# Kernel tuning notes

Hardware: AMD Instinct MI355X
Metric: run time of the kernel (lower is better)

## Reference

```python
import jax, jax.numpy as jnp
import numpy as np

_EPS = 1e-6
B, N, W, R, NW = 64, 1024, 64, 4, 1


def _cosine_weights(memory, keys, strengths):
    # memory: [B,N,W], keys: [B,H,W], strengths: [B,H] -> [B,H,N]
    dot = jnp.einsum('bhw,bnw->bhn', keys, memory)
    mem_norm = jnp.sqrt(jnp.sum(memory * memory, axis=-1) + _EPS)  # [B,N]
    key_norm = jnp.sqrt(jnp.sum(keys * keys, axis=-1) + _EPS)      # [B,H]
    sim = dot / (key_norm[:, :, None] * mem_norm[:, None, :] + _EPS)
    sharp = sim * jax.nn.softplus(strengths)[:, :, None]
    return jax.nn.softmax(sharp, axis=-1)


def _allocation(usage):
    # usage: [B,N] -> allocation weights [B,N] (DNC sort-based free-list)
    usage = _EPS + (1.0 - _EPS) * usage
    nonusage = 1.0 - usage
    sorted_nonusage, indices = jax.lax.top_k(nonusage, N)
    sorted_usage = 1.0 - sorted_nonusage
    prod_excl = jnp.concatenate(
        [jnp.ones_like(sorted_usage[:, :1]), jnp.cumprod(sorted_usage[:, :-1], axis=-1)], axis=-1)
    sorted_alloc = sorted_nonusage * prod_excl
    inv_perm = jnp.argsort(indices, axis=-1)  # batch_invert_permutation
    return jnp.take_along_axis(sorted_alloc, inv_perm, axis=-1)  # batch_gather


def _forward(memory, prev_read_weights, prev_write_weights, prev_usage, prev_link,
             prev_precedence, read_keys, read_strengths, write_keys, write_strengths,
             write_vectors, erase_vectors, free_gate, alloc_gate, write_gate, read_mode):
    # ---- usage update (Freeness.call); prev write weights are stop-gradient'd ----
    ww = jax.lax.stop_gradient(prev_write_weights)
    agg_write = 1.0 - jnp.prod(1.0 - ww, axis=1)                       # [B,N]
    usage = prev_usage + (1.0 - prev_usage) * agg_write
    phi = jnp.prod(1.0 - free_gate[:, :, None] * prev_read_weights, axis=1)
    usage = usage * phi
    # ---- write weights: content + allocation ----
    write_content = _cosine_weights(memory, write_keys, write_strengths)  # [B,NW,N]
    wg = alloc_gate * write_gate                                          # [B,NW]
    allocs = []
    u = usage
    for i in range(NW):  # fixed small head loop
        a = _allocation(u)
        allocs.append(a)
        u = u + (1.0 - u) * wg[:, i:i + 1] * a
    alloc_w = jnp.stack(allocs, axis=1)                                   # [B,NW,N]
    ag = alloc_gate[:, :, None]
    write_weights = write_gate[:, :, None] * (ag * alloc_w + (1.0 - ag) * write_content)
    # ---- erase + write memory ----
    reset = jnp.prod(1.0 - write_weights[:, :, :, None] * erase_vectors[:, :, None, :], axis=1)
    memory_new = memory * reset + jnp.einsum('bwn,bwk->bnk', write_weights, write_vectors)
    # ---- temporal link matrix update ----
    wi = write_weights[:, :, :, None]   # [B,NW,N,1]
    wj = write_weights[:, :, None, :]   # [B,NW,1,N]
    new_link = (1.0 - wi - wj) * prev_link + wi * prev_precedence[:, :, None, :]
    link = new_link * (1.0 - jnp.eye(N, dtype=memory.dtype))[None, None]  # zero diagonal
    # (precedence update, part of new state; not needed for read_words output)
    precedence = (1.0 - jnp.sum(write_weights, axis=-1, keepdims=True)) * prev_precedence + write_weights
    del precedence
    # ---- read weights: content + directional (forward/backward along link) ----
    read_content = _cosine_weights(memory_new, read_keys, read_strengths)   # [B,R,N]
    fwd_w = jnp.einsum('brm,bwnm->brwn', prev_read_weights, link)           # adjoint_b=True
    bwd_w = jnp.einsum('brm,bwmn->brwn', prev_read_weights, link)
    mode = jax.nn.softmax(read_mode, axis=-1)                                # [B,R,2*NW+1]
    backward_mode = mode[:, :, :NW]
    forward_mode = mode[:, :, NW:2 * NW]
    content_mode = mode[:, :, 2 * NW]
    read_weights = (content_mode[:, :, None] * read_content
                    + jnp.einsum('brw,brwn->brn', forward_mode, fwd_w)
                    + jnp.einsum('brw,brwn->brn', backward_mode, bwd_w))
    read_words = jnp.einsum('brn,bnw->brw', read_weights, memory_new)        # [B,R,W]
    return read_words


def setup_inputs() -> dict:
    key = jax.random.key(0)
    ks = jax.random.split(key, 16)
    rn = lambda k, s: jax.random.normal(k, s, jnp.float32)
    ru = lambda k, s: jax.random.uniform(k, s, dtype=jnp.float32)
    return {
        'memory': rn(ks[0], (B, N, W)),
        'prev_read_weights': ru(ks[1], (B, R, N)),
        'prev_write_weights': ru(ks[2], (B, NW, N)),
        'prev_usage': ru(ks[3], (B, N)),
        'prev_link': ru(ks[4], (B, NW, N, N)),
        'prev_precedence': ru(ks[5], (B, NW, N)),
        'read_keys': rn(ks[6], (B, R, W)),
        'read_strengths': rn(ks[7], (B, R)),
        'write_keys': rn(ks[8], (B, NW, W)),
        'write_strengths': rn(ks[9], (B, NW)),
        'write_vectors': rn(ks[10], (B, NW, W)),
        'erase_vectors': ru(ks[11], (B, NW, W)),
        'free_gate': ru(ks[12], (B, R)),
        'alloc_gate': ru(ks[13], (B, NW)),
        'write_gate': ru(ks[14], (B, NW)),
        'read_mode': rn(ks[15], (B, R, 2 * NW + 1)),
    }


def reference(memory, prev_read_weights, prev_write_weights, prev_usage, prev_link,
              prev_precedence, read_keys, read_strengths, write_keys, write_strengths,
              write_vectors, erase_vectors, free_gate, alloc_gate, write_gate, read_mode):
    return _forward(memory, prev_read_weights, prev_write_weights, prev_usage, prev_link,
                    prev_precedence, read_keys, read_strengths, write_keys, write_strengths,
                    write_vectors, erase_vectors, free_gate, alloc_gate, write_gate, read_mode)
```

## Files before the change

### kernel.cpp

```cpp
#include <hip/hip_runtime.h>
#include <cmath>

#define NN 1024
#define BB 64
#define WD 64
#define RR 4

constexpr float EPSF = 1e-6f;

__device__ __forceinline__ float softplusf(float x) {
    return fmaxf(x, 0.f) + log1pf(expf(-fabsf(x)));
}

__device__ __forceinline__ float block_sum(float v, float* red, float* bc) {
#pragma unroll
    for (int o = 1; o < 64; o <<= 1) v += __shfl_xor(v, o, 64);
    const int wid = threadIdx.x >> 6, lane = threadIdx.x & 63;
    if (lane == 0) red[wid] = v;
    __syncthreads();
    if (wid == 0) {
        float x = (lane < 16) ? red[lane] : 0.f;
#pragma unroll
        for (int o = 1; o < 16; o <<= 1) x += __shfl_xor(x, o, 64);
        if (lane == 0) bc[0] = x;
    }
    __syncthreads();
    return bc[0];
}

__device__ __forceinline__ float block_max(float v, float* red, float* bc) {
#pragma unroll
    for (int o = 1; o < 64; o <<= 1) v = fmaxf(v, __shfl_xor(v, o, 64));
    const int wid = threadIdx.x >> 6, lane = threadIdx.x & 63;
    if (lane == 0) red[wid] = v;
    __syncthreads();
    if (wid == 0) {
        float x = (lane < 16) ? red[lane] : -INFINITY;
#pragma unroll
        for (int o = 1; o < 16; o <<= 1) x = fmaxf(x, __shfl_xor(x, o, 64));
        if (lane == 0) bc[0] = x;
    }
    __syncthreads();
    return bc[0];
}

__device__ __forceinline__ float4 block_sum4(float4 v, float4* red, float4* bc) {
#pragma unroll
    for (int o = 1; o < 64; o <<= 1) {
        v.x += __shfl_xor(v.x, o, 64); v.y += __shfl_xor(v.y, o, 64);
        v.z += __shfl_xor(v.z, o, 64); v.w += __shfl_xor(v.w, o, 64);
    }
    const int wid = threadIdx.x >> 6, lane = threadIdx.x & 63;
    if (lane == 0) red[wid] = v;
    __syncthreads();
    if (wid == 0) {
        float4 x;
        if (lane < 16) x = red[lane];
        else { x.x = 0.f; x.y = 0.f; x.z = 0.f; x.w = 0.f; }
#pragma unroll
        for (int o = 1; o < 16; o <<= 1) {
            x.x += __shfl_xor(x.x, o, 64); x.y += __shfl_xor(x.y, o, 64);
            x.z += __shfl_xor(x.z, o, 64); x.w += __shfl_xor(x.w, o, 64);
        }
        if (lane == 0) bc[0] = x;
    }
    __syncthreads();
    return bc[0];
}

__device__ __forceinline__ float4 block_max4(float4 v, float4* red, float4* bc) {
#pragma unroll
    for (int o = 1; o < 64; o <<= 1) {
        v.x = fmaxf(v.x, __shfl_xor(v.x, o, 64)); v.y = fmaxf(v.y, __shfl_xor(v.y, o, 64));
        v.z = fmaxf(v.z, __shfl_xor(v.z, o, 64)); v.w = fmaxf(v.w, __shfl_xor(v.w, o, 64));
    }
    const int wid = threadIdx.x >> 6, lane = threadIdx.x & 63;
    if (lane == 0) red[wid] = v;
    __syncthreads();
    if (wid == 0) {
        float4 x;
        if (lane < 16) x = red[lane];
        else { x.x = -INFINITY; x.y = -INFINITY; x.z = -INFINITY; x.w = -INFINITY; }
#pragma unroll
        for (int o = 1; o < 16; o <<= 1) {
            x.x = fmaxf(x.x, __shfl_xor(x.x, o, 64)); x.y = fmaxf(x.y, __shfl_xor(x.y, o, 64));
            x.z = fmaxf(x.z, __shfl_xor(x.z, o, 64)); x.w = fmaxf(x.w, __shfl_xor(x.w, o, 64));
        }
        if (lane == 0) bc[0] = x;
    }
    __syncthreads();
    return bc[0];
}

__global__ __launch_bounds__(1024) void prep_kernel(
    const float* __restrict__ memory, const float* __restrict__ prw,
    const float* __restrict__ pww, const float* __restrict__ pusage,
    const float* __restrict__ pprec,
    const float* __restrict__ rkeys_g, const float* __restrict__ rstr_g,
    const float* __restrict__ wkeys_g, const float* __restrict__ wstr_g,
    const float* __restrict__ wvec_g, const float* __restrict__ evec_g,
    const float* __restrict__ fg_g, const float* __restrict__ ag_g,
    const float* __restrict__ wg_g,
    float* __restrict__ wwG, float* __restrict__ rcG,
    float* __restrict__ SrpG, float* __restrict__ SuwwG)
{
    __shared__ float wkey[WD], wvecS[WD], evecS[WD], rkey[RR * WD];
    __shared__ float skey[NN];
    __shared__ int   sidx[NN];
    __shared__ float pArr[NN], wcArr[NN], allocArr[NN];
    __shared__ float red1[16], bc1[1];
    __shared__ float4 red4[16], bc4[1];

    const int b = blockIdx.x, tid = threadIdx.x, n = tid;

    if (tid < WD) {
        wkey[tid]  = wkeys_g[b * WD + tid];
        wvecS[tid] = wvec_g[b * WD + tid];
        evecS[tid] = evec_g[b * WD + tid];
    } else if (tid >= 128 && tid < 128 + RR * WD) {
        int k = tid - 128;
        rkey[k] = rkeys_g[b * RR * WD + k];
    }
    __syncthreads();

    float ur[RR];
#pragma unroll
    for (int r = 0; r < RR; ++r) ur[r] = prw[((size_t)b * RR + r) * NN + n];
    const float pw = pww[b * NN + n];
    const float pu = pusage[b * NN + n];
    float usage = pu + (1.f - pu) * pw;
    float phi = 1.f;
#pragma unroll
    for (int r = 0; r < RR; ++r) phi *= (1.f - fg_g[b * RR + r] * ur[r]);
    usage *= phi;

    const float* mrow = memory + ((size_t)b * NN + n) * WD;
    float dot = 0.f, nrm = 0.f, knrm = 0.f;
#pragma unroll 4
    for (int w4 = 0; w4 < WD / 4; ++w4) {
        const float4 m = *(const float4*)(mrow + w4 * 4);
        const float4 k = *(const float4*)(wkey + w4 * 4);
        dot  += m.x * k.x + m.y * k.y + m.z * k.z + m.w * k.w;
        nrm  += m.x * m.x + m.y * m.y + m.z * m.z + m.w * m.w;
        knrm += k.x * k.x + k.y * k.y + k.z * k.z + k.w * k.w;
    }
    const float sim = dot / (sqrtf(knrm + EPSF) * sqrtf(nrm + EPSF) + EPSF);
    const float sharp = sim * softplusf(wstr_g[b]);
    const float mxw = block_max(sharp, red1, bc1);
    const float exw = expf(sharp - mxw);
    const float smw = block_sum(exw, red1, bc1);
    wcArr[n] = exw / smw;

    const float ue = EPSF + (1.f - EPSF) * usage;
    skey[n] = 1.f - ue;
    sidx[n] = n;
    __syncthreads();
    for (int k = 2; k <= NN; k <<= 1) {
        for (int j = k >> 1; j > 0; j >>= 1) {
            const int ixj = tid ^ j;
            if (ixj > tid) {
                const float ka = skey[tid], kb = skey[ixj];
                const int ia = sidx[tid], ib = sidx[ixj];
                const bool precBA = (kb > ka) || (kb == ka && ib < ia);
                const bool precAB = (ka > kb) || (ka == kb && ia < ib);
                const bool dosw = ((tid & k) == 0) ? precBA : precAB;
                if (dosw) { skey[tid] = kb; skey[ixj] = ka; sidx[tid] = ib; sidx[ixj] = ia; }
            }
            __syncthreads();
        }
    }
    pArr[n] = (n == 0) ? 1.f : (1.f - skey[n - 1]);
    __syncthreads();
    for (int off = 1; off < NN; off <<= 1) {
        const float t = (n >= off) ? pArr[n - off] : 1.f;
        __syncthreads();
        pArr[n] *= t;
        __syncthreads();
    }
    allocArr[sidx[n]] = skey[n] * pArr[n];
    __syncthreads();

    const float agv = ag_g[b], wgv = wg_g[b];
    const float ww = wgv * (agv * allocArr[n] + (1.f - agv) * wcArr[n]);
    wwG[b * NN + n] = ww;

    float rdot0 = 0, rdot1 = 0, rdot2 = 0, rdot3 = 0, nn2 = 0;
    float rk0 = 0, rk1 = 0, rk2 = 0, rk3 = 0;
#pragma unroll 4
    for (int w4 = 0; w4 < WD / 4; ++w4) {
        const float4 m = *(const float4*)(mrow + w4 * 4);
        const float4 e = *(const float4*)(evecS + w4 * 4);
        const float4 v = *(const float4*)(wvecS + w4 * 4);
        float4 mn_;
        mn_.x = m.x * (1.f - ww * e.x) + ww * v.x;
        mn_.y = m.y * (1.f - ww * e.y) + ww * v.y;
        mn_.z = m.z * (1.f - ww * e.z) + ww * v.z;
        mn_.w = m.w * (1.f - ww * e.w) + ww * v.w;
        nn2 += mn_.x * mn_.x + mn_.y * mn_.y + mn_.z * mn_.z + mn_.w * mn_.w;
        const float4 k0 = *(const float4*)(rkey + 0 * WD + w4 * 4);
        const float4 k1 = *(const float4*)(rkey + 1 * WD + w4 * 4);
        const float4 k2 = *(const float4*)(rkey + 2 * WD + w4 * 4);
        const float4 k3 = *(const float4*)(rkey + 3 * WD + w4 * 4);
        rdot0 += k0.x * mn_.x + k0.y * mn_.y + k0.z * mn_.z + k0.w * mn_.w;
        rdot1 += k1.x * mn_.x + k1.y * mn_.y + k1.z * mn_.z + k1.w * mn_.w;
        rdot2 += k2.x * mn_.x + k2.y * mn_.y + k2.z * mn_.z + k2.w * mn_.w;
        rdot3 += k3.x * mn_.x + k3.y * mn_.y + k3.z * mn_.z + k3.w * mn_.w;
        rk0 += k0.x * k0.x + k0.y * k0.y + k0.z * k0.z + k0.w * k0.w;
        rk1 += k1.x * k1.x + k1.y * k1.y + k1.z * k1.z + k1.w * k1.w;
        rk2 += k2.x * k2.x + k2.y * k2.y + k2.z * k2.z + k2.w * k2.w;
        rk3 += k3.x * k3.x + k3.y * k3.y + k3.z * k3.z + k3.w * k3.w;
    }
    const float mnn = sqrtf(nn2 + EPSF);
    float4 sharp4;
    sharp4.x = rdot0 / (sqrtf(rk0 + EPSF) * mnn + EPSF) * softplusf(rstr_g[b * RR + 0]);
    sharp4.y = rdot1 / (sqrtf(rk1 + EPSF) * mnn + EPSF) * softplusf(rstr_g[b * RR + 1]);
    sharp4.z = rdot2 / (sqrtf(rk2 + EPSF) * mnn + EPSF) * softplusf(rstr_g[b * RR + 2]);
    sharp4.w = rdot3 / (sqrtf(rk3 + EPSF) * mnn + EPSF) * softplusf(rstr_g[b * RR + 3]);
    const float4 mx4 = block_max4(sharp4, red4, bc4);
    float4 e4;
    e4.x = expf(sharp4.x - mx4.x); e4.y = expf(sharp4.y - mx4.y);
    e4.z = expf(sharp4.z - mx4.z); e4.w = expf(sharp4.w - mx4.w);
    const float4 s4 = block_sum4(e4, red4, bc4);
    rcG[((size_t)b * RR + 0) * NN + n] = e4.x / s4.x;
    rcG[((size_t)b * RR + 1) * NN + n] = e4.y / s4.y;
    rcG[((size_t)b * RR + 2) * NN + n] = e4.z / s4.z;
    rcG[((size_t)b * RR + 3) * NN + n] = e4.w / s4.w;

    const float prec_n = pprec[b * NN + n];
    float4 sp4, sw4;
    sp4.x = ur[0] * prec_n; sp4.y = ur[1] * prec_n; sp4.z = ur[2] * prec_n; sp4.w = ur[3] * prec_n;
    const float4 SrpV = block_sum4(sp4, red4, bc4);
    sw4.x = ur[0] * ww; sw4.y = ur[1] * ww; sw4.z = ur[2] * ww; sw4.w = ur[3] * ww;
    const float4 SuwwV = block_sum4(sw4, red4, bc4);
    if (tid == 0) {
        SrpG[b * RR + 0] = SrpV.x; SrpG[b * RR + 1] = SrpV.y;
        SrpG[b * RR + 2] = SrpV.z; SrpG[b * RR + 3] = SrpV.w;
        SuwwG[b * RR + 0] = SuwwV.x; SuwwG[b * RR + 1] = SuwwV.y;
        SuwwG[b * RR + 2] = SuwwV.z; SuwwG[b * RR + 3] = SuwwV.w;
    }
}

__global__ __launch_bounds__(256) void link_kernel(
    const float* __restrict__ L, const float* __restrict__ prw,
    const float* __restrict__ wwG,
    float* __restrict__ rowU, float* __restrict__ rowV,
    float* __restrict__ colU, float* __restrict__ colV)
{
    __shared__ float uL[RR * NN];
    __shared__ float uwL[RR * NN];
    __shared__ float tile[64 * 68];

    const int b = blockIdx.y;
    const int n0 = blockIdx.x * 64;
    const int t = threadIdx.x;
    const int lane = t & 63;
    const int wid = t >> 6;

    for (int k = t; k < RR * NN; k += 256) {
        const float u = prw[(size_t)b * RR * NN + k];
        uL[k] = u;
        uwL[k] = u * wwG[b * NN + (k & (NN - 1))];
    }
    __syncthreads();

    const float* Lb = L + (size_t)b * NN * NN;
    float fuA = 0.f, fvA = 0.f;

    for (int tIdx = 0; tIdx < 16; ++tIdx) {
        const int m0 = tIdx * 64;
#pragma unroll
        for (int k = 0; k < 4; ++k) {
            const int f4 = t + k * 256;
            const int row = f4 >> 4, c4 = f4 & 15;
            const float4 v = *(const float4*)&Lb[(size_t)(n0 + row) * NN + m0 + c4 * 4];
            *(float4*)&tile[row * 68 + c4 * 4] = v;
        }
        __syncthreads();

#pragma unroll 4
        for (int g = 0; g < 16; ++g) {
            const float4 v  = *(const float4*)&tile[lane * 68 + g * 4];
            const float4 u  = *(const float4*)&uL[wid * NN + m0 + g * 4];
            const float4 uw = *(const float4*)&uwL[wid * NN + m0 + g * 4];
            fuA += v.x * u.x + v.y * u.y + v.z * u.z + v.w * u.w;
            fvA += v.x * uw.x + v.y * uw.y + v.z * uw.z + v.w * uw.w;
        }

        float cu = 0.f, cv = 0.f;
#pragma unroll 4
        for (int n4 = 0; n4 < 16; ++n4) {
            const float4 u  = *(const float4*)&uL[wid * NN + n0 + n4 * 4];
            const float4 uw = *(const float4*)&uwL[wid * NN + n0 + n4 * 4];
            const float v0 = tile[(n4 * 4 + 0) * 68 + lane];
            const float v1 = tile[(n4 * 4 + 1) * 68 + lane];
            const float v2 = tile[(n4 * 4 + 2) * 68 + lane];
            const float v3 = tile[(n4 * 4 + 3) * 68 + lane];
            cu += v0 * u.x + v1 * u.y + v2 * u.z + v3 * u.w;
            cv += v0 * uw.x + v1 * uw.y + v2 * uw.z + v3 * uw.w;
        }
        unsafeAtomicAdd(&colU[((size_t)b * RR + wid) * NN + m0 + lane], cu);
        unsafeAtomicAdd(&colV[((size_t)b * RR + wid) * NN + m0 + lane], cv);
        __syncthreads();
    }
    rowU[((size_t)b * RR + wid) * NN + n0 + lane] = fuA;
    rowV[((size_t)b * RR + wid) * NN + n0 + lane] = fvA;
}

__global__ __launch_bounds__(256) void combine_kernel(
    const float* __restrict__ memory, const float* __restrict__ prw,
    const float* __restrict__ pprec, const float* __restrict__ L,
    const float* __restrict__ evec_g, const float* __restrict__ wvec_g,
    const float* __restrict__ rmode_g,
    const float* __restrict__ wwG, const float* __restrict__ rcG,
    const float* __restrict__ rowU, const float* __restrict__ rowV,
    const float* __restrict__ colU, const float* __restrict__ colV,
    const float* __restrict__ SrpG, const float* __restrict__ SuwwG,
    float* __restrict__ out)
{
    __shared__ float rwL[RR][256];
    __shared__ float wwS[256];

    const int b = blockIdx.y;
    const int n0 = blockIdx.x * 256;
    const int t = threadIdx.x;
    const int n = n0 + t;

    const float wwn = wwG[b * NN + n];
    wwS[t] = wwn;
    const float prec_n = pprec[b * NN + n];
    const float diag = L[(size_t)b * NN * NN + (size_t)n * (NN + 1)];

#pragma unroll
    for (int r = 0; r < RR; ++r) {
        const size_t idx = ((size_t)b * RR + r) * NN + n;
        const float un = prw[idx];
        const float rc = rcG[idx];
        const float ru = rowU[idx], rv = rowV[idx];
        const float cuv = colU[idx], cvv = colV[idx];
        const float Srp = SrpG[b * RR + r], Suww = SuwwG[b * RR + r];
        const float corr = un * (1.f - 2.f * wwn) * diag;
        const float fwd = (1.f - wwn) * ru - rv - corr + wwn * (Srp - un * prec_n);
        const float bwd = (1.f - wwn) * cuv - cvv - corr + prec_n * (Suww - un * wwn);
        const float m0 = rmode_g[((size_t)b * RR + r) * 3 + 0];
        const float m1 = rmode_g[((size_t)b * RR + r) * 3 + 1];
        const float m2 = rmode_g[((size_t)b * RR + r) * 3 + 2];
        const float mx = fmaxf(m0, fmaxf(m1, m2));
        const float e0 = expf(m0 - mx), e1 = expf(m1 - mx), e2 = expf(m2 - mx);
        const float inv = 1.f / (e0 + e1 + e2);
        rwL[r][t] = (e2 * inv) * rc + (e1 * inv) * fwd + (e0 * inv) * bwd;
    }
    __syncthreads();

    const int r = t >> 6, w = t & 63;
    const float ev = evec_g[b * WD + w], wv = wvec_g[b * WD + w];
    float acc = 0.f;
    const float* mb = memory + ((size_t)b * NN + n0) * WD;
#pragma unroll 8
    for (int i = 0; i < 256; ++i) {
        const float m = mb[(size_t)i * WD + w];
        const float wwi = wwS[i];
        const float mn_ = m * (1.f - wwi * ev) + wwi * wv;
        acc += rwL[r][i] * mn_;
    }
    unsafeAtomicAdd(&out[((size_t)b * RR + r) * WD + w], acc);
}

extern "C" void kernel_launch(void* const* d_in, const int* in_sizes, int n_in,
                              void* d_out, int out_size, void* d_ws, size_t ws_size,
                              hipStream_t stream) {
    const float* memory = (const float*)d_in[0];
    const float* prw    = (const float*)d_in[1];
    const float* pww    = (const float*)d_in[2];
    const float* pusage = (const float*)d_in[3];
    const float* plink  = (const float*)d_in[4];
    const float* pprec  = (const float*)d_in[5];
    const float* rkeys  = (const float*)d_in[6];
    const float* rstr   = (const float*)d_in[7];
    const float* wkeys  = (const float*)d_in[8];
    const float* wstr   = (const float*)d_in[9];
    const float* wvec   = (const float*)d_in[10];
    const float* evec   = (const float*)d_in[11];
    const float* fg     = (const float*)d_in[12];
    const float* ag     = (const float*)d_in[13];
    const float* wg     = (const float*)d_in[14];
    const float* rmode  = (const float*)d_in[15];

    float* ws = (float*)d_ws;
    const size_t BN  = (size_t)BB * NN;
    const size_t BRN = (size_t)BB * RR * NN;
    float* wwG  = ws;
    float* rcG  = wwG + BN;
    float* rowU = rcG + BRN;
    float* rowV = rowU + BRN;
    float* colU = rowV + BRN;
    float* colV = colU + BRN;
    float* Srp  = colV + BRN;
    float* Suww = Srp + (size_t)BB * RR;

    hipMemsetAsync(colU, 0, 2 * BRN * sizeof(float), stream);
    hipMemsetAsync(d_out, 0, (size_t)out_size * sizeof(float), stream);

    prep_kernel<<<BB, 1024, 0, stream>>>(memory, prw, pww, pusage, pprec,
                                         rkeys, rstr, wkeys, wstr, wvec, evec,
                                         fg, ag, wg, wwG, rcG, Srp, Suww);
    link_kernel<<<dim3(16, BB), 256, 0, stream>>>(plink, prw, wwG,
                                                  rowU, rowV, colU, colV);
    combine_kernel<<<dim3(4, BB), 256, 0, stream>>>(memory, prw, pprec, plink,
                                                    evec, wvec, rmode,
                                                    wwG, rcG, rowU, rowV, colU, colV,
                                                    Srp, Suww, (float*)d_out);
}
```

Baseline: 600.0 us.

## Split link kernel across column quarters with register prefetch and smaller LDS

The link kernel now splits each row block into four column ranges, raising the grid from 16 to 64 blocks per batch. It shrinks the u/uw shared buffers to the slices each block needs, and uses atomics for the row partial sums (the buffers are now zeroed by memset). It also prefetches the next L tile into registers while computing on the current one. It reorganises column sums as float4 partials with a cross-lane shuffle reduction, and precomputes u*ww in the prep kernel. The combine kernel is split into more, smaller blocks for parallelism. The cost is more atomics and extra global traffic for uwG.

```diff
diff --git a/kernel.cpp b/kernel.cpp
--- a/kernel.cpp
+++ b/kernel.cpp
@@ -101,7 +101,7 @@
     const float* __restrict__ wvec_g, const float* __restrict__ evec_g,
     const float* __restrict__ fg_g, const float* __restrict__ ag_g,
     const float* __restrict__ wg_g,
-    float* __restrict__ wwG, float* __restrict__ rcG,
+    float* __restrict__ wwG, float* __restrict__ uwG, float* __restrict__ rcG,
     float* __restrict__ SrpG, float* __restrict__ SuwwG)
 {
     __shared__ float wkey[WD], wvecS[WD], evecS[WD], rkey[RR * WD];
@@ -183,6 +183,9 @@
     const float agv = ag_g[b], wgv = wg_g[b];
     const float ww = wgv * (agv * allocArr[n] + (1.f - agv) * wcArr[n]);
     wwG[b * NN + n] = ww;
+#pragma unroll
+    for (int r = 0; r < RR; ++r)
+        uwG[((size_t)b * RR + r) * NN + n] = ur[r] * ww;
 
     float rdot0 = 0, rdot1 = 0, rdot2 = 0, rdot3 = 0, nn2 = 0;
     float rk0 = 0, rk1 = 0, rk2 = 0, rk3 = 0;
@@ -240,70 +243,113 @@
     }
 }
 
-__global__ __launch_bounds__(256) void link_kernel(
-    const float* __restrict__ L, const float* __restrict__ prw,
-    const float* __restrict__ wwG,
+__global__ __launch_bounds__(256, 4) void link_kernel(
+    const float* __restrict__ L, const float* __restrict__ uG,
+    const float* __restrict__ uwG,
     float* __restrict__ rowU, float* __restrict__ rowV,
     float* __restrict__ colU, float* __restrict__ colV)
 {
-    __shared__ float uL[RR * NN];
-    __shared__ float uwL[RR * NN];
+    __shared__ float uRow[RR * 256];
+    __shared__ float uwRow[RR * 256];
+    __shared__ float uCol[RR * 64];
+    __shared__ float uwCol[RR * 64];
     __shared__ float tile[64 * 68];
 
     const int b = blockIdx.y;
-    const int n0 = blockIdx.x * 64;
+    const int bx = blockIdx.x;
+    const int n0 = (bx >> 2) * 64;
+    const int mBase = (bx & 3) * 256;
     const int t = threadIdx.x;
     const int lane = t & 63;
     const int wid = t >> 6;
 
-    for (int k = t; k < RR * NN; k += 256) {
-        const float u = prw[(size_t)b * RR * NN + k];
-        uL[k] = u;
-        uwL[k] = u * wwG[b * NN + (k & (NN - 1))];
-    }
-    __syncthreads();
-
-    const float* Lb = L + (size_t)b * NN * NN;
+#pragma unroll
+    for (int k = 0; k < 4; ++k) {
+        const int kk = t + (k << 8);
+        const int r = kk >> 8, m = kk & 255;
+        const size_t gi = ((size_t)b * RR + r) * NN + mBase + m;
+        uRow[kk]  = uG[gi];
+        uwRow[kk] = uwG[gi];
+    }
+    {
+        const int r = t >> 6, i = t & 63;
+        const size_t gi = ((size_t)b * RR + r) * NN + n0 + i;
+        uCol[t]  = uG[gi];
+        uwCol[t] = uwG[gi];
+    }
+
+    const float* Lb = L + (size_t)b * NN * NN + (size_t)n0 * NN + mBase;
+    const int srow = t >> 4;
+    const int sc4  = (t & 15) << 2;
+
+    float4 pre[4];
+#pragma unroll
+    for (int k = 0; k < 4; ++k)
+        pre[k] = *(const float4*)&Lb[(size_t)(srow + (k << 4)) * NN + sc4];
+#pragma unroll
+    for (int k = 0; k < 4; ++k)
+        *(float4*)&tile[(srow + (k << 4)) * 68 + sc4] = pre[k];
+
     float fuA = 0.f, fvA = 0.f;
-
-    for (int tIdx = 0; tIdx < 16; ++tIdx) {
-        const int m0 = tIdx * 64;
-#pragma unroll
-        for (int k = 0; k < 4; ++k) {
-            const int f4 = t + k * 256;
-            const int row = f4 >> 4, c4 = f4 & 15;
-            const float4 v = *(const float4*)&Lb[(size_t)(n0 + row) * NN + m0 + c4 * 4];
-            *(float4*)&tile[row * 68 + c4 * 4] = v;
-        }
+    const int q = lane >> 4;
+    const int c16 = (lane & 15) << 2;
+
+#pragma unroll
+    for (int tt = 0; tt < 4; ++tt) {
         __syncthreads();
-
-#pragma unroll 4
+        if (tt < 3) {
+#pragma unroll
+            for (int k = 0; k < 4; ++k)
+                pre[k] = *(const float4*)&Lb[(size_t)(srow + (k << 4)) * NN + ((tt + 1) << 6) + sc4];
+        }
+
+#pragma unroll
         for (int g = 0; g < 16; ++g) {
-            const float4 v  = *(const float4*)&tile[lane * 68 + g * 4];
-            const float4 u  = *(const float4*)&uL[wid * NN + m0 + g * 4];
-            const float4 uw = *(const float4*)&uwL[wid * NN + m0 + g * 4];
+            const float4 v  = *(const float4*)&tile[lane * 68 + (g << 2)];
+            const float4 u  = *(const float4*)&uRow[(wid << 8) + (tt << 6) + (g << 2)];
+            const float4 uw = *(const float4*)&uwRow[(wid << 8) + (tt << 6) + (g << 2)];
             fuA += v.x * u.x + v.y * u.y + v.z * u.z + v.w * u.w;
             fvA += v.x * uw.x + v.y * uw.y + v.z * uw.z + v.w * uw.w;
         }
 
-        float cu = 0.f, cv = 0.f;
-#pragma unroll 4
+        float4 cu4 = {0.f, 0.f, 0.f, 0.f}, cv4 = {0.f, 0.f, 0.f, 0.f};
+#pragma unroll
         for (int n4 = 0; n4 < 16; ++n4) {
-            const float4 u  = *(const float4*)&uL[wid * NN + n0 + n4 * 4];
-            const float4 uw = *(const float4*)&uwL[wid * NN + n0 + n4 * 4];
-            const float v0 = tile[(n4 * 4 + 0) * 68 + lane];
-            const float v1 = tile[(n4 * 4 + 1) * 68 + lane];
-            const float v2 = tile[(n4 * 4 + 2) * 68 + lane];
-            const float v3 = tile[(n4 * 4 + 3) * 68 + lane];
-            cu += v0 * u.x + v1 * u.y + v2 * u.z + v3 * u.w;
-            cv += v0 * uw.x + v1 * uw.y + v2 * uw.z + v3 * uw.w;
-        }
-        unsafeAtomicAdd(&colU[((size_t)b * RR + wid) * NN + m0 + lane], cu);
-        unsafeAtomicAdd(&colV[((size_t)b * RR + wid) * NN + m0 + lane], cv);
+            const int row = (n4 << 2) + q;
+            const float4 v = *(const float4*)&tile[row * 68 + c16];
+            const float uv  = uCol[(wid << 6) + row];
+            const float uwv = uwCol[(wid << 6) + row];
+            cu4.x += uv * v.x;  cu4.y += uv * v.y;  cu4.z += uv * v.z;  cu4.w += uv * v.w;
+            cv4.x += uwv * v.x; cv4.y += uwv * v.y; cv4.z += uwv * v.z; cv4.w += uwv * v.w;
+        }
+#pragma unroll
+        for (int off = 16; off < 64; off <<= 1) {
+            cu4.x += __shfl_xor(cu4.x, off, 64); cu4.y += __shfl_xor(cu4.y, off, 64);
+            cu4.z += __shfl_xor(cu4.z, off, 64); cu4.w += __shfl_xor(cu4.w, off, 64);
+            cv4.x += __shfl_xor(cv4.x, off, 64); cv4.y += __shfl_xor(cv4.y, off, 64);
+            cv4.z += __shfl_xor(cv4.z, off, 64); cv4.w += __shfl_xor(cv4.w, off, 64);
+        }
+        if (lane < 16) {
+            const size_t cb = ((size_t)b * RR + wid) * NN + mBase + (tt << 6) + (lane << 2);
+            unsafeAtomicAdd(&colU[cb + 0], cu4.x);
+            unsafeAtomicAdd(&colU[cb + 1], cu4.y);
+            unsafeAtomicAdd(&colU[cb + 2], cu4.z);
+            unsafeAtomicAdd(&colU[cb + 3], cu4.w);
+            unsafeAtomicAdd(&colV[cb + 0], cv4.x);
+            unsafeAtomicAdd(&colV[cb + 1], cv4.y);
+            unsafeAtomicAdd(&colV[cb + 2], cv4.z);
+            unsafeAtomicAdd(&colV[cb + 3], cv4.w);
+        }
+
         __syncthreads();
-    }
-    rowU[((size_t)b * RR + wid) * NN + n0 + lane] = fuA;
-    rowV[((size_t)b * RR + wid) * NN + n0 + lane] = fvA;
+        if (tt < 3) {
+#pragma unroll
+            for (int k = 0; k < 4; ++k)
+                *(float4*)&tile[(srow + (k << 4)) * 68 + sc4] = pre[k];
+        }
+    }
+    unsafeAtomicAdd(&rowU[((size_t)b * RR + wid) * NN + n0 + lane], fuA);
+    unsafeAtomicAdd(&rowV[((size_t)b * RR + wid) * NN + n0 + lane], fvA);
 }
 
 __global__ __launch_bounds__(256) void combine_kernel(
@@ -317,21 +363,21 @@
     const float* __restrict__ SrpG, const float* __restrict__ SuwwG,
     float* __restrict__ out)
 {
-    __shared__ float rwL[RR][256];
-    __shared__ float wwS[256];
+    __shared__ float rwL[RR][64];
+    __shared__ float wwS[64];
 
     const int b = blockIdx.y;
-    const int n0 = blockIdx.x * 256;
+    const int n0 = blockIdx.x * 64;
     const int t = threadIdx.x;
-    const int n = n0 + t;
+    const int r = t >> 6, i = t & 63;
+    const int n = n0 + i;
 
     const float wwn = wwG[b * NN + n];
-    wwS[t] = wwn;
+    if (r == 0) wwS[i] = wwn;
     const float prec_n = pprec[b * NN + n];
     const float diag = L[(size_t)b * NN * NN + (size_t)n * (NN + 1)];
 
-#pragma unroll
-    for (int r = 0; r < RR; ++r) {
+    {
         const size_t idx = ((size_t)b * RR + r) * NN + n;
         const float un = prw[idx];
         const float rc = rcG[idx];
@@ -347,20 +393,19 @@
         const float mx = fmaxf(m0, fmaxf(m1, m2));
         const float e0 = expf(m0 - mx), e1 = expf(m1 - mx), e2 = expf(m2 - mx);
         const float inv = 1.f / (e0 + e1 + e2);
-        rwL[r][t] = (e2 * inv) * rc + (e1 * inv) * fwd + (e0 * inv) * bwd;
-    }
-    __syncthreads();
-
-    const int r = t >> 6, w = t & 63;
+        rwL[r][i] = (e2 * inv) * rc + (e1 * inv) * fwd + (e0 * inv) * bwd;
+    }
+    __syncthreads();
+
+    const int w = i;
     const float ev = evec_g[b * WD + w], wv = wvec_g[b * WD + w];
     float acc = 0.f;
     const float* mb = memory + ((size_t)b * NN + n0) * WD;
 #pragma unroll 8
-    for (int i = 0; i < 256; ++i) {
-        const float m = mb[(size_t)i * WD + w];
-        const float wwi = wwS[i];
-        const float mn_ = m * (1.f - wwi * ev) + wwi * wv;
-        acc += rwL[r][i] * mn_;
+    for (int k = 0; k < 64; ++k) {
+        const float m = mb[(size_t)k * WD + w];
+        const float wwi = wwS[k];
+        acc += rwL[r][k] * (m * (1.f - wwi * ev) + wwi * wv);
     }
     unsafeAtomicAdd(&out[((size_t)b * RR + r) * WD + w], acc);
 }
@@ -390,23 +435,24 @@
     const size_t BRN = (size_t)BB * RR * NN;
     float* wwG  = ws;
     float* rcG  = wwG + BN;
-    float* rowU = rcG + BRN;
+    float* uwG  = rcG + BRN;
+    float* rowU = uwG + BRN;
     float* rowV = rowU + BRN;
     float* colU = rowV + BRN;
     float* colV = colU + BRN;
     float* Srp  = colV + BRN;
     float* Suww = Srp + (size_t)BB * RR;
 
-    hipMemsetAsync(colU, 0, 2 * BRN * sizeof(float), stream);
+    hipMemsetAsync(rowU, 0, 4 * BRN * sizeof(float), stream);
     hipMemsetAsync(d_out, 0, (size_t)out_size * sizeof(float), stream);
 
     prep_kernel<<<BB, 1024, 0, stream>>>(memory, prw, pww, pusage, pprec,
                                          rkeys, rstr, wkeys, wstr, wvec, evec,
-                                         fg, ag, wg, wwG, rcG, Srp, Suww);
-    link_kernel<<<dim3(16, BB), 256, 0, stream>>>(plink, prw, wwG,
+                                         fg, ag, wg, wwG, uwG, rcG, Srp, Suww);
+    link_kernel<<<dim3(64, BB), 256, 0, stream>>>(plink, prw, uwG,
                                                   rowU, rowV, colU, colV);
-    combine_kernel<<<dim3(4, BB), 256, 0, stream>>>(memory, prw, pprec, plink,
-                                                    evec, wvec, rmode,
-                                                    wwG, rcG, rowU, rowV, colU, colV,
-                                                    Srp, Suww, (float*)d_out);
-}
+    combine_kernel<<<dim3(16, BB), 256, 0, stream>>>(memory, prw, pprec, plink,
+                                                     evec, wvec, rmode,
+                                                     wwG, rcG, rowU, rowV, colU, colV,
+                                                     Srp, Suww, (float*)d_out);
+}
```

After: 1.748 ms. +191.4%, slower.
